# Optimization experiments

Measured on AMD Instinct MI355X. Metric: run time of the kernel, lower is better.

## Reference

```python
import jax, jax.numpy as jnp
import numpy as np

EPS = 1e-5

def _ste(x, q):
    # straight-through estimator: forward=q, backward=identity
    return x + jax.lax.stop_gradient(q - x)

def act_quant(x):
    # per-token int8 absmax quantization (BitNet b1.58 style), fake-quantized
    scale = 127.0 / jnp.clip(jnp.max(jnp.abs(x), axis=-1, keepdims=True), EPS)
    q = jnp.clip(jnp.round(x * scale), -128.0, 127.0) / scale
    return _ste(x, q)

def weight_quant(w):
    # ternary {-1,0,1} weights scaled by mean absolute value
    s = jnp.clip(jnp.mean(jnp.abs(w)), EPS)
    q = jnp.clip(jnp.round(w / s), -1.0, 1.0) * s
    return _ste(w, q)

def bit_linear(x, w):
    # x: [..., in], w: [out, in]
    return jnp.einsum('bsi,oi->bso', act_quant(x), weight_quant(w))

def setup_inputs() -> dict:
    key = jax.random.key(0)
    k1, k2, k3 = jax.random.split(key, 3)
    d_model, hidden = 2048, 4 * 2048
    x = jax.random.normal(k1, (4, 2048, d_model), dtype=jnp.float32)
    w1 = jax.random.normal(k2, (hidden, d_model), dtype=jnp.float32) * 0.02
    w2 = jax.random.normal(k3, (d_model, hidden), dtype=jnp.float32) * 0.02
    return {"x": x, "w1": w1, "w2": w2}

def reference(x, w1, w2):
    h = bit_linear(x, w1)            # [B, S, 4*d]
    h = jax.nn.gelu(h, approximate=False)  # exact erf GELU (nn.GELU default)
    return bit_linear(h, w2)         # [B, S, d]
```

## Files before the change

kernel.cpp:

```cpp
#include <hip/hip_runtime.h>
#include <hip/hip_bf16.h>
#include <hip/hip_fp16.h>
#include <stdint.h>

#define TPB 256
#define EPSF 1e-5f

using i32x4 = __attribute__((ext_vector_type(4))) int;


__device__ __forceinline__ void gload16(const void* g, void* l) {
    __builtin_amdgcn_global_load_lds(
        (__attribute__((address_space(1))) void*)g,
        (__attribute__((address_space(3))) void*)l,
        16, 0, 0);
}

__device__ __forceinline__ float wave_reduce_sum(float v) {
#pragma unroll
    for (int off = 32; off > 0; off >>= 1) v += __shfl_down(v, off, 64);
    return v;
}

__device__ __forceinline__ float wave_reduce_max(float v) {
#pragma unroll
    for (int off = 32; off > 0; off >>= 1) v = fmaxf(v, __shfl_down(v, off, 64));
    return v;
}

__device__ __forceinline__ int q8(float f, float scale, float lo, float hi) {
    return (int)fminf(fmaxf(rintf(f * scale), lo), hi);
}

__device__ __forceinline__ float gelu_fast(float x) {
    float x2 = x * x;
    float u = x * (0.7978845608f + 0.0356774081f * x2);
    float e = exp2f(u * -2.8853900817779268f);
    return x * __builtin_amdgcn_rcpf(1.0f + e);
}


__global__ void abssum2(const float* __restrict__ w1, const float* __restrict__ w2,
                        int n4, float* __restrict__ part) {
    const bool second = blockIdx.x >= 2048;
    const float4* w4 = (const float4*)(second ? w2 : w1);
    const int b = blockIdx.x & 2047;
    float acc = 0.f;
    for (int i = b * TPB + threadIdx.x; i < n4; i += 2048 * TPB) {
        float4 v = w4[i];
        acc += fabsf(v.x) + fabsf(v.y) + fabsf(v.z) + fabsf(v.w);
    }
    acc = wave_reduce_sum(acc);
    __shared__ float sh[4];
    if ((threadIdx.x & 63) == 0) sh[threadIdx.x >> 6] = acc;
    __syncthreads();
    if (threadIdx.x == 0) part[blockIdx.x] = sh[0] + sh[1] + sh[2] + sh[3];
}

__global__ void finalize_scales(const float* __restrict__ part,
                                float* __restrict__ scales, float inv_n) {
    float a = 0.f, b = 0.f;
    for (int i = threadIdx.x; i < 2048; i += TPB) { a += part[i]; b += part[i + 2048]; }
    a = wave_reduce_sum(a);
    b = wave_reduce_sum(b);
    __shared__ float sa[4], sb[4];
    if ((threadIdx.x & 63) == 0) { sa[threadIdx.x >> 6] = a; sb[threadIdx.x >> 6] = b; }
    __syncthreads();
    if (threadIdx.x == 0) {
        scales[0] = fmaxf((sa[0] + sa[1] + sa[2] + sa[3]) * inv_n, EPSF);
        scales[1] = fmaxf((sb[0] + sb[1] + sb[2] + sb[3]) * inv_n, EPSF);
    }
}


__global__ void quant_w_i8(const float* __restrict__ w,
                           signed char* __restrict__ wq,
                           const float* __restrict__ scales, int sidx, int n4) {
    const float inv = 1.0f / scales[sidx];
    const float4* w4 = (const float4*)w;
    unsigned* oq = (unsigned*)wq;
    for (int i = blockIdx.x * TPB + threadIdx.x; i < n4; i += gridDim.x * TPB) {
        float4 v = w4[i];
        unsigned p = ((unsigned)(q8(v.x, inv, -1.f, 1.f) & 0xff)) |
                     ((unsigned)(q8(v.y, inv, -1.f, 1.f) & 0xff) << 8) |
                     ((unsigned)(q8(v.z, inv, -1.f, 1.f) & 0xff) << 16) |
                     ((unsigned)(q8(v.w, inv, -1.f, 1.f) & 0xff) << 24);
        oq[i] = p;
    }
}


template <int NF4>
__global__ void quant_x_i8(const float* __restrict__ in,
                           signed char* __restrict__ outq,
                           float* __restrict__ dq, int cols) {
    const long long row = blockIdx.x;
    const float4* r4 = (const float4*)(in + row * (long long)cols);
    float4 v[NF4];
    float mx = 0.f;
#pragma unroll
    for (int j = 0; j < NF4; ++j) {
        v[j] = r4[threadIdx.x + TPB * j];
        mx = fmaxf(mx, fmaxf(fmaxf(fabsf(v[j].x), fabsf(v[j].y)),
                             fmaxf(fabsf(v[j].z), fabsf(v[j].w))));
    }
    mx = wave_reduce_max(mx);
    __shared__ float sh[4];
    __shared__ float res;
    if ((threadIdx.x & 63) == 0) sh[threadIdx.x >> 6] = mx;
    __syncthreads();
    if (threadIdx.x == 0) res = fmaxf(fmaxf(sh[0], sh[1]), fmaxf(sh[2], sh[3]));
    __syncthreads();
    const float clipped = fmaxf(res, EPSF);
    const float scale = 127.f / clipped;
    if (threadIdx.x == 0) dq[row] = clipped / 127.f;
    unsigned* oq = (unsigned*)(outq + row * (long long)cols);
#pragma unroll
    for (int j = 0; j < NF4; ++j) {
        unsigned p = ((unsigned)(q8(v[j].x, scale, -128.f, 127.f) & 0xff)) |
                     ((unsigned)(q8(v[j].y, scale, -128.f, 127.f) & 0xff) << 8) |
                     ((unsigned)(q8(v[j].z, scale, -128.f, 127.f) & 0xff) << 16) |
                     ((unsigned)(q8(v[j].w, scale, -128.f, 127.f) & 0xff) << 24);
        oq[threadIdx.x + TPB * j] = p;
    }
}


template <int NJ>
__global__ void quant_h_i8(const unsigned short* __restrict__ h,
                           signed char* __restrict__ outq,
                           float* __restrict__ dq, int cols) {
    const long long row = blockIdx.x;
    const unsigned short* rp = h + row * (long long)cols;
    uint4 v[NJ];
    float mx = 0.f;
#pragma unroll
    for (int j = 0; j < NJ; ++j) {
        v[j] = *(const uint4*)(rp + (threadIdx.x + TPB * j) * 8);
        const unsigned* u = (const unsigned*)&v[j];
#pragma unroll
        for (int e = 0; e < 4; ++e) {
            float2 f2 = __half22float2(*(const __half2*)&u[e]);
            mx = fmaxf(mx, fmaxf(fabsf(f2.x), fabsf(f2.y)));
        }
    }
    mx = wave_reduce_max(mx);
    __shared__ float sh[4];
    __shared__ float res;
    if ((threadIdx.x & 63) == 0) sh[threadIdx.x >> 6] = mx;
    __syncthreads();
    if (threadIdx.x == 0) res = fmaxf(fmaxf(sh[0], sh[1]), fmaxf(sh[2], sh[3]));
    __syncthreads();
    const float clipped = fmaxf(res, EPSF);
    const float scale = 127.f / clipped;
    if (threadIdx.x == 0) dq[row] = clipped / 127.f;
    uint2* oq = (uint2*)(outq + row * (long long)cols);
#pragma unroll
    for (int j = 0; j < NJ; ++j) {
        const unsigned* u = (const unsigned*)&v[j];
        unsigned o[2] = {0, 0};
#pragma unroll
        for (int e = 0; e < 4; ++e) {
            float2 f2 = __half22float2(*(const __half2*)&u[e]);
            unsigned b0 = (unsigned)(q8(f2.x, scale, -128.f, 127.f) & 0xff);
            unsigned b1 = (unsigned)(q8(f2.y, scale, -128.f, 127.f) & 0xff);
            o[e >> 1] |= (b0 | (b1 << 8)) << ((e & 1) * 16);
        }
        oq[threadIdx.x + TPB * j] = *(uint2*)o;
    }
}


__device__ __forceinline__ void stage_half(const char* Xb, long long rowB, int prow,
                                           int tk, char* dst, int tid, int cbs) {
    const long long gc = (long long)tk * 128 + cbs;
    const int r = tid >> 3;
    gload16(Xb + (long long)(prow + r) * rowB + gc, dst + tid * 16);
    gload16(Xb + (long long)(prow + 64 + r) * rowB + gc, dst + 8192 + tid * 16);
}

#define QUAD(MB, NB)                                                            \
    _Pragma("unroll") for (int mi = 0; mi < 4; ++mi)                            \
    _Pragma("unroll") for (int ni = 0; ni < 2; ++ni)                            \
    _Pragma("unroll") for (int ks = 0; ks < 2; ++ks)                            \
        acc[(MB)*4 + mi][(NB)*2 + ni] = __builtin_amdgcn_mfma_i32_16x16x64_i8(  \
            aq[mi][ks], bq[(NB)*2 + ni][ks], acc[(MB)*4 + mi][(NB)*2 + ni], 0, 0, 0);

#define READ_A(base_mi)                                                         \
    _Pragma("unroll") for (int mi = 0; mi < 4; ++mi) {                          \
        const char* p = cur + aoff + ((mi + (base_mi)) * 16 + l15) * 128;       \
        aq[mi][0] = *(const i32x4*)(p + acb0);                                  \
        aq[mi][1] = *(const i32x4*)(p + acb1);                                  \
    }
#define READ_B(n0i, n1i)                                                        \
    _Pragma("unroll") for (int ni = (n0i); ni < (n1i); ++ni) {                  \
        const char* p = cur + boff + (ni * 16 + l15) * 128;                     \
        bq[ni][0] = *(const i32x4*)(p + acb0);                                  \
        bq[ni][1] = *(const i32x4*)(p + acb1);                                  \
    }

#define EMIT1(MLO, MHI, M0V)                                                    \
    _Pragma("unroll") for (int mi = (MLO); mi < (MHI); ++mi) {                  \
        _Pragma("unroll") for (int r = 0; r < 4; ++r) {                         \
            const long long m = (M0V) + wr * 128 + mi * 16 + l4 * 4 + r;        \
            const float f = dq[m] * s;                                          \
            _Pragma("unroll") for (int ni = 0; ni < 4; ++ni) {                  \
                const long long n = n0 + wc * 64 + ni * 16 + l15;               \
                float v = gelu_fast((float)acc[mi][ni][r] * f);                 \
                __half hh = __float2half(v);                                    \
                C[m * (long long)N + n] = *(const unsigned short*)&hh;          \
                acc[mi][ni][r] = 0;                                             \
            }                                                                   \
        }                                                                       \
    }


__global__ __launch_bounds__(512, 2) void gemm1p(
    const signed char* __restrict__ A, const signed char* __restrict__ B,
    unsigned short* __restrict__ C, int N, int K,
    const float* __restrict__ dq, const float* __restrict__ scales, int ntile) {
    __shared__ __align__(16) char lds[131072];

    const int tid = threadIdx.x;
    const int lane = tid & 63;
    const int wid = tid >> 6;
    const int wr = wid >> 2;
    const int wc = wid & 3;

    const unsigned orig = blockIdx.y * gridDim.x + blockIdx.x;
    const unsigned xk = orig & 7, j = orig >> 3;
    const unsigned bx = (xk & 3) * 8 + (j & 7);
    const unsigned byg = (xk >> 2) * 4 + (j >> 3);

    const int n0 = (int)bx * 256;
    const long long rb = (long long)K;
    const char* Ab = (const char*)A;
    const char* Bb = (const char*)B;

    const int NTT = ntile << 4;

    const int cbs = (((tid & 7) ^ ((tid >> 3) & 7)) << 4);
    const int l15 = lane & 15, l4 = lane >> 4;
    const int swz = (lane & 7) << 4;
    const int acb0 = (l4 * 16) ^ swz;
    const int acb1 = (64 + l4 * 16) ^ swz;
    const int aoff = wr * 16384;
    const int boff = 32768 + (wc >> 1) * 16384 + (wc & 1) * 8192;

    i32x4 acc[8][4] = {};
    i32x4 aq[4][2], bq[4][2];

    auto mrow = [&](int v) -> int { return ((int)byg * ntile + (v >> 4)) * 256; };

    stage_half(Bb, rb, n0, 0, lds + 32768, tid, cbs);
    stage_half(Bb, rb, n0 + 128, 0, lds + 32768 + 16384, tid, cbs);
    stage_half(Ab, rb, mrow(0), 0, lds + 0, tid, cbs);
    stage_half(Ab, rb, mrow(0) + 128, 0, lds + 16384, tid, cbs);
    stage_half(Bb, rb, n0, 1, lds + 65536 + 32768, tid, cbs);
    stage_half(Bb, rb, n0 + 128, 1, lds + 65536 + 32768 + 16384, tid, cbs);
    stage_half(Ab, rb, mrow(1), 1, lds + 65536, tid, cbs);
    asm volatile("s_waitcnt vmcnt(6)" ::: "memory");
    __builtin_amdgcn_sched_barrier(0);
    __builtin_amdgcn_s_barrier();

    const float s = scales[0];

    for (int vt = 0; vt < NTT; ++vt) {
        char* cur = lds + ((vt & 1) << 16);
        char* nxt = lds + (((vt + 1) & 1) << 16);
        const bool s1 = (vt + 1) < NTT;
        const bool s2 = (vt + 2) < NTT;
        const int kk = vt & 15;
        const int k1 = (vt + 1) & 15;
        const int k2 = (vt + 2) & 15;

        READ_A(0);
        READ_B(0, 2);
        if (s1) stage_half(Ab, rb, mrow(vt + 1) + 128, k1, nxt + 16384, tid, cbs);
        if (kk == 0 && vt > 0) { EMIT1(4, 8, mrow(vt - 1)); }
        __builtin_amdgcn_s_setprio(1);
        QUAD(0, 0);
        __builtin_amdgcn_s_setprio(0);
        __builtin_amdgcn_s_barrier();

        READ_B(2, 4);
        if (s2) stage_half(Bb, rb, n0, k2, cur + 32768, tid, cbs);
        __builtin_amdgcn_s_setprio(1);
        QUAD(0, 1);
        __builtin_amdgcn_s_setprio(0);
        __builtin_amdgcn_s_barrier();

        READ_A(4);
        if (s2) stage_half(Bb, rb, n0 + 128, k2, cur + 32768 + 16384, tid, cbs);
        if (kk == 15) { EMIT1(0, 4, mrow(vt)); }
        __builtin_amdgcn_s_setprio(1);
        QUAD(1, 0);
        __builtin_amdgcn_s_setprio(0);
        __builtin_amdgcn_s_barrier();

        if (s2) stage_half(Ab, rb, mrow(vt + 2), k2, cur, tid, cbs);
        __builtin_amdgcn_s_setprio(1);
        QUAD(1, 1);
        __builtin_amdgcn_s_setprio(0);
        if (s2) { asm volatile("s_waitcnt vmcnt(6)" ::: "memory"); }
        else    { asm volatile("s_waitcnt vmcnt(0)" ::: "memory"); }
        __builtin_amdgcn_sched_barrier(0);
        __builtin_amdgcn_s_barrier();
    }

    { EMIT1(4, 8, mrow(NTT - 1)); }
}


#define EMIT2(MLO, MHI)                                                         \
    _Pragma("unroll") for (int mi = (MLO); mi < (MHI); ++mi) {                  \
        _Pragma("unroll") for (int r = 0; r < 4; ++r) {                         \
            const long long m = M0 + wr * 128 + mi * 16 + l4 * 4 + r;           \
            const float f = dq[m] * s;                                          \
            _Pragma("unroll") for (int ni = 0; ni < 4; ++ni) {                  \
                const long long n = N0 + wc * 64 + ni * 16 + l15;               \
                __builtin_nontemporal_store(                                    \
                    (float)acc[mi][ni][r] * f, C + m * (long long)N + n);       \
            }                                                                   \
        }                                                                       \
    }

__global__ __launch_bounds__(512, 2) void gemm2k(
    const signed char* __restrict__ A, const signed char* __restrict__ B,
    float* __restrict__ C, int N, int K,
    const float* __restrict__ dq, const float* __restrict__ scales) {
    __shared__ __align__(16) char lds[131072];

    const int tid = threadIdx.x;
    const int lane = tid & 63;
    const int wid = tid >> 6;
    const int wr = wid >> 2;
    const int wc = wid & 3;

    const unsigned gx = gridDim.x;
    unsigned lin = blockIdx.y * gx + blockIdx.x;
    const unsigned qq = (gx * gridDim.y) >> 3;
    lin = (lin & 7) * qq + (lin >> 3);
    const unsigned bx = lin % gx;
    const unsigned by = lin / gx;

    const long long M0 = (long long)by * 256;
    const long long N0 = (long long)bx * 256;
    const long long rb = (long long)K;
    const char* Ab = (const char*)A + M0 * rb;
    const char* Bb = (const char*)B + N0 * rb;
    const int nt = K >> 7;

    const int cbs = (((tid & 7) ^ ((tid >> 3) & 7)) << 4);
    const int l15 = lane & 15, l4 = lane >> 4;
    const int swz = (lane & 7) << 4;
    const int acb0 = (l4 * 16) ^ swz;
    const int acb1 = (64 + l4 * 16) ^ swz;
    const int aoff = wr * 16384;
    const int boff = 32768 + (wc >> 1) * 16384 + (wc & 1) * 8192;

    i32x4 acc[8][4] = {};
    i32x4 aq[4][2], bq[4][2];

    stage_half(Bb, rb, 0,   0, lds + 32768,         tid, cbs);
    stage_half(Bb, rb, 128, 0, lds + 32768 + 16384, tid, cbs);
    stage_half(Ab, rb, 0,   0, lds + 0,             tid, cbs);
    stage_half(Ab, rb, 128, 0, lds + 16384,         tid, cbs);
    stage_half(Bb, rb, 0,   1, lds + 65536 + 32768,         tid, cbs);
    stage_half(Bb, rb, 128, 1, lds + 65536 + 32768 + 16384, tid, cbs);
    stage_half(Ab, rb, 0,   1, lds + 65536,                 tid, cbs);
    asm volatile("s_waitcnt vmcnt(6)" ::: "memory");
    __builtin_amdgcn_sched_barrier(0);
    __builtin_amdgcn_s_barrier();

    const float s = scales[1];

    for (int t = 0; t < nt; ++t) {
        char* cur = lds + ((t & 1) << 16);
        char* nxt = lds + (((t + 1) & 1) << 16);
        const bool s1 = (t + 1) < nt;
        const bool s2 = (t + 2) < nt;

        READ_A(0);
        READ_B(0, 2);
        if (s1) stage_half(Ab, rb, 128, t + 1, nxt + 16384, tid, cbs);
        __builtin_amdgcn_s_setprio(1);
        QUAD(0, 0);
        __builtin_amdgcn_s_setprio(0);
        __builtin_amdgcn_s_barrier();

        READ_B(2, 4);
        if (s2) stage_half(Bb, rb, 0, t + 2, cur + 32768, tid, cbs);
        __builtin_amdgcn_s_setprio(1);
        QUAD(0, 1);
        __builtin_amdgcn_s_setprio(0);
        __builtin_amdgcn_s_barrier();

        READ_A(4);
        if (s2) stage_half(Bb, rb, 128, t + 2, cur + 32768 + 16384, tid, cbs);
        if (t == nt - 1) { EMIT2(0, 4); }
        __builtin_amdgcn_s_setprio(1);
        QUAD(1, 0);
        __builtin_amdgcn_s_setprio(0);
        __builtin_amdgcn_s_barrier();

        if (s2) stage_half(Ab, rb, 0, t + 2, cur, tid, cbs);
        __builtin_amdgcn_s_setprio(1);
        QUAD(1, 1);
        __builtin_amdgcn_s_setprio(0);
        if (s2) { asm volatile("s_waitcnt vmcnt(6)" ::: "memory"); }
        else    { asm volatile("s_waitcnt vmcnt(0)" ::: "memory"); }
        __builtin_amdgcn_sched_barrier(0);
        __builtin_amdgcn_s_barrier();
    }

    { EMIT2(4, 8); }
}


extern "C" void kernel_launch(void* const* d_in, const int* in_sizes, int n_in,
                              void* d_out, int out_size, void* d_ws, size_t ws_size,
                              hipStream_t stream) {
    (void)n_in; (void)out_size;
    const float* x  = (const float*)d_in[0];
    const float* w1 = (const float*)d_in[1];
    const float* w2 = (const float*)d_in[2];
    float* out = (float*)d_out;

    const int D = 2048, H = 8192;
    const long long M = (long long)in_sizes[0] / D;

    char* base = (char*)d_ws;
    size_t off = 0;
    auto alloc = [&](size_t bytes) -> char* {
        char* r = base + off;
        off = (off + bytes + 255) & ~(size_t)255;
        return r;
    };

    const bool fullM = ws_size >= (size_t)236 * 1024 * 1024;
    const long long MC = fullM ? M : M / 2;

    float* part = (float*)alloc(4096 * 4);
    float* scales = (float*)alloc(256);
    float* dqx = (float*)alloc((size_t)M * 4);
    float* dqh = (float*)alloc((size_t)M * 4);
    signed char* wq = (signed char*)alloc((size_t)H * D);
    signed char* xq = (signed char*)alloc((size_t)M * D);
    signed char* hq = (signed char*)alloc((size_t)M * H);
    unsigned short* hf = (unsigned short*)alloc((size_t)MC * H * 2);

    const int nw4 = H * D / 4;
    abssum2<<<4096, TPB, 0, stream>>>(w1, w2, nw4, part);
    finalize_scales<<<1, TPB, 0, stream>>>(part, scales, 1.0f / (float)(H * D));
    quant_w_i8<<<2048, TPB, 0, stream>>>(w1, wq, scales, 0, nw4);
    quant_x_i8<2><<<(int)M, TPB, 0, stream>>>(x, xq, dqx, D);

    if (fullM) {
        gemm1p<<<dim3(32, 8), 512, 0, stream>>>(xq, wq, hf, H, D, dqx, scales, 4);
        quant_h_i8<4><<<(int)M, TPB, 0, stream>>>(hf, hq, dqh, H);
    } else {
        for (int g = 0; g < 2; ++g) {
            const long long m0 = g * MC;
            gemm1p<<<dim3(32, 8), 512, 0, stream>>>(
                xq + m0 * D, wq, hf, H, D, dqx + m0, scales, 2);
            quant_h_i8<4><<<(int)MC, TPB, 0, stream>>>(hf, hq + m0 * H, dqh + m0, H);
        }
    }

    quant_w_i8<<<2048, TPB, 0, stream>>>(w2, wq, scales, 1, nw4);

    gemm2k<<<dim3(D / 256, (int)(M / 256)), 512, 0, stream>>>(
        hq, wq, out, D, H, dqh, scales);
}
```

Baseline: 357.6 us.

## Software-pipeline LDS fragment reads ahead of MFMA phases with explicit lgkmcnt waits

Restructures the main loops of both int8 GEMM kernels so the LDS register-fragment reads for the next phase are issued before the current MFMA block. The first A/B fragments of the next tile are prefetched at the end of each iteration, and explicit lgkmcnt waits replace the implicit dependencies. The B-tile global stages are grouped together and the vmcnt/barrier placement is moved to fit the new ordering. This aims to hide LDS read latency behind MFMA work, at the cost of more register pressure and tighter correctness reasoning about buffer reuse around barriers.

```diff
diff --git a/kernel.cpp b/kernel.cpp
--- a/kernel.cpp
+++ b/kernel.cpp
@@ -186,18 +186,21 @@
         acc[(MB)*4 + mi][(NB)*2 + ni] = __builtin_amdgcn_mfma_i32_16x16x64_i8(  \
             aq[mi][ks], bq[(NB)*2 + ni][ks], acc[(MB)*4 + mi][(NB)*2 + ni], 0, 0, 0);
 
-#define READ_A(base_mi)                                                         \
+#define READ_A(BUF, base_mi)                                                    \
     _Pragma("unroll") for (int mi = 0; mi < 4; ++mi) {                          \
-        const char* p = cur + aoff + ((mi + (base_mi)) * 16 + l15) * 128;       \
+        const char* p = (BUF) + aoff + ((mi + (base_mi)) * 16 + l15) * 128;     \
         aq[mi][0] = *(const i32x4*)(p + acb0);                                  \
         aq[mi][1] = *(const i32x4*)(p + acb1);                                  \
     }
-#define READ_B(n0i, n1i)                                                        \
+#define READ_B(BUF, n0i, n1i)                                                   \
     _Pragma("unroll") for (int ni = (n0i); ni < (n1i); ++ni) {                  \
-        const char* p = cur + boff + (ni * 16 + l15) * 128;                     \
+        const char* p = (BUF) + boff + (ni * 16 + l15) * 128;                   \
         bq[ni][0] = *(const i32x4*)(p + acb0);                                  \
         bq[ni][1] = *(const i32x4*)(p + acb1);                                  \
     }
+
+#define LGKM(N) do { asm volatile("s_waitcnt lgkmcnt(" #N ")" ::: "memory");    \
+                     __builtin_amdgcn_sched_barrier(0); } while (0)
 
 #define EMIT1(MLO, MHI, M0V)                                                    \
     _Pragma("unroll") for (int mi = (MLO); mi < (MHI); ++mi) {                  \
@@ -262,6 +265,8 @@
     asm volatile("s_waitcnt vmcnt(6)" ::: "memory");
     __builtin_amdgcn_sched_barrier(0);
     __builtin_amdgcn_s_barrier();
+    READ_A(lds, 0);
+    READ_B(lds, 0, 2);
 
     const float s = scales[0];
 
@@ -274,38 +279,45 @@
         const int k1 = (vt + 1) & 15;
         const int k2 = (vt + 2) & 15;
 
-        READ_A(0);
-        READ_B(0, 2);
         if (s1) stage_half(Ab, rb, mrow(vt + 1) + 128, k1, nxt + 16384, tid, cbs);
+        READ_B(cur, 2, 4);
         if (kk == 0 && vt > 0) { EMIT1(4, 8, mrow(vt - 1)); }
+        __builtin_amdgcn_s_barrier();
+        LGKM(4);
         __builtin_amdgcn_s_setprio(1);
         QUAD(0, 0);
         __builtin_amdgcn_s_setprio(0);
-        __builtin_amdgcn_s_barrier();
-
-        READ_B(2, 4);
-        if (s2) stage_half(Bb, rb, n0, k2, cur + 32768, tid, cbs);
+
+        __builtin_amdgcn_s_barrier();
+        LGKM(0);
         __builtin_amdgcn_s_setprio(1);
         QUAD(0, 1);
         __builtin_amdgcn_s_setprio(0);
-        __builtin_amdgcn_s_barrier();
-
-        READ_A(4);
-        if (s2) stage_half(Bb, rb, n0 + 128, k2, cur + 32768 + 16384, tid, cbs);
+
+        if (s2) {
+            stage_half(Bb, rb, n0, k2, cur + 32768, tid, cbs);
+            stage_half(Bb, rb, n0 + 128, k2, cur + 32768 + 16384, tid, cbs);
+        }
+        READ_A(cur, 4);
         if (kk == 15) { EMIT1(0, 4, mrow(vt)); }
+        __builtin_amdgcn_s_barrier();
+        LGKM(0);
         __builtin_amdgcn_s_setprio(1);
         QUAD(1, 0);
         __builtin_amdgcn_s_setprio(0);
-        __builtin_amdgcn_s_barrier();
-
-        if (s2) stage_half(Ab, rb, mrow(vt + 2), k2, cur, tid, cbs);
-        __builtin_amdgcn_s_setprio(1);
-        QUAD(1, 1);
-        __builtin_amdgcn_s_setprio(0);
-        if (s2) { asm volatile("s_waitcnt vmcnt(6)" ::: "memory"); }
+
+        if (s2) { asm volatile("s_waitcnt vmcnt(4)" ::: "memory"); }
         else    { asm volatile("s_waitcnt vmcnt(0)" ::: "memory"); }
         __builtin_amdgcn_sched_barrier(0);
         __builtin_amdgcn_s_barrier();
+        if (s2) stage_half(Ab, rb, mrow(vt + 2), k2, cur, tid, cbs);
+        __builtin_amdgcn_s_setprio(1);
+        QUAD(1, 1);
+        __builtin_amdgcn_s_setprio(0);
+        if (s1) {
+            READ_A(nxt, 0);
+            READ_B(nxt, 0, 2);
+        }
     }
 
     { EMIT1(4, 8, mrow(NTT - 1)); }
@@ -372,6 +384,8 @@
     asm volatile("s_waitcnt vmcnt(6)" ::: "memory");
     __builtin_amdgcn_sched_barrier(0);
     __builtin_amdgcn_s_barrier();
+    READ_A(lds, 0);
+    READ_B(lds, 0, 2);
 
     const float s = scales[1];
 
@@ -381,37 +395,44 @@
         const bool s1 = (t + 1) < nt;
         const bool s2 = (t + 2) < nt;
 
-        READ_A(0);
-        READ_B(0, 2);
         if (s1) stage_half(Ab, rb, 128, t + 1, nxt + 16384, tid, cbs);
+        READ_B(cur, 2, 4);
+        __builtin_amdgcn_s_barrier();
+        LGKM(4);
         __builtin_amdgcn_s_setprio(1);
         QUAD(0, 0);
         __builtin_amdgcn_s_setprio(0);
-        __builtin_amdgcn_s_barrier();
-
-        READ_B(2, 4);
-        if (s2) stage_half(Bb, rb, 0, t + 2, cur + 32768, tid, cbs);
+
+        __builtin_amdgcn_s_barrier();
+        LGKM(0);
         __builtin_amdgcn_s_setprio(1);
         QUAD(0, 1);
         __builtin_amdgcn_s_setprio(0);
-        __builtin_amdgcn_s_barrier();
-
-        READ_A(4);
-        if (s2) stage_half(Bb, rb, 128, t + 2, cur + 32768 + 16384, tid, cbs);
+
+        if (s2) {
+            stage_half(Bb, rb, 0, t + 2, cur + 32768, tid, cbs);
+            stage_half(Bb, rb, 128, t + 2, cur + 32768 + 16384, tid, cbs);
+        }
+        READ_A(cur, 4);
         if (t == nt - 1) { EMIT2(0, 4); }
+        __builtin_amdgcn_s_barrier();
+        LGKM(0);
         __builtin_amdgcn_s_setprio(1);
         QUAD(1, 0);
         __builtin_amdgcn_s_setprio(0);
-        __builtin_amdgcn_s_barrier();
-
-        if (s2) stage_half(Ab, rb, 0, t + 2, cur, tid, cbs);
-        __builtin_amdgcn_s_setprio(1);
-        QUAD(1, 1);
-        __builtin_amdgcn_s_setprio(0);
-        if (s2) { asm volatile("s_waitcnt vmcnt(6)" ::: "memory"); }
+
+        if (s2) { asm volatile("s_waitcnt vmcnt(4)" ::: "memory"); }
         else    { asm volatile("s_waitcnt vmcnt(0)" ::: "memory"); }
         __builtin_amdgcn_sched_barrier(0);
         __builtin_amdgcn_s_barrier();
+        if (s2) stage_half(Ab, rb, 0, t + 2, cur, tid, cbs);
+        __builtin_amdgcn_s_setprio(1);
+        QUAD(1, 1);
+        __builtin_amdgcn_s_setprio(0);
+        if (s1) {
+            READ_A(nxt, 0);
+            READ_B(nxt, 0, 2);
+        }
     }
 
     { EMIT2(4, 8); }
```

After: 357.6 us. No clear change (-0.0%).
